# Kernel optimization log

Hardware: AMD Instinct MI355X
Metric: run time of the kernel (lower is better)

## Reference

```python
import jax, jax.numpy as jnp
import numpy as np

B, N = 16, 16          # batch, boxes per image
H, W = 640, 640        # image size
PH, PW = 300, 300      # learned patch size
MIN_AREA = 60.0
MAX_ANG = 20.0 * np.pi / 180.0


def setup_inputs() -> dict:
    key = jax.random.key(0)
    k1, k2, k3 = jax.random.split(key, 3)
    images = jax.random.uniform(k1, (B, H, W, 3), jnp.float32, -1.0, 1.0)
    patch = jax.random.uniform(k2, (PH, PW, 3), jnp.float32, -1.0, 1.0)
    kb1, kb2, kb3 = jax.random.split(k3, 3)
    ymin = jax.random.uniform(kb1, (B, N), jnp.float32, 0.0, H - 220.0)
    xmin = jax.random.uniform(kb2, (B, N), jnp.float32, 0.0, W - 220.0)
    hw = jax.random.uniform(kb3, (B, N, 2), jnp.float32, 100.0, 200.0)
    boxes = jnp.stack([ymin, xmin, ymin + hw[..., 0], xmin + hw[..., 1]], axis=-1)
    scale = jnp.float32(0.4)
    return {"boxes": boxes, "images": images, "patch": patch, "scale": scale}


def _bilinear(img, ys, xs):
    # img [Ph,Pw,3]; ys,xs [H,W] continuous source coords -> [H,W,3]
    Ph, Pw = img.shape[0], img.shape[1]
    y0 = jnp.floor(ys)
    x0 = jnp.floor(xs)
    wy = (ys - y0)[..., None]
    wx = (xs - x0)[..., None]
    y0i = jnp.clip(y0.astype(jnp.int32), 0, Ph - 1)
    y1i = jnp.clip(y0i + 1, 0, Ph - 1)
    x0i = jnp.clip(x0.astype(jnp.int32), 0, Pw - 1)
    x1i = jnp.clip(x0i + 1, 0, Pw - 1)
    v00 = img[y0i, x0i]
    v01 = img[y0i, x1i]
    v10 = img[y1i, x0i]
    v11 = img[y1i, x1i]
    return v00 * (1 - wy) * (1 - wx) + v01 * (1 - wy) * wx + v10 * wy * (1 - wx) + v11 * wy * wx


def _per_image(img, boxes_i, patch, scale, key):
    # random_print_adjust: per-channel affine jitter of the patch
    kw, kb, kloop = jax.random.split(key, 3)
    w = jax.random.normal(kw, (1, 1, 3), jnp.float32) * 0.1 + 0.5
    b = jax.random.normal(kb, (1, 1, 3), jnp.float32) * 0.01
    p = jnp.clip(w * patch + b, -1.0, 1.0)
    # BrightnessMatcher: shift patch mean brightness to match the image
    p = jnp.clip(p + (jnp.mean(img) - jnp.mean(p)), -1.0, 1.0)

    oimg = img
    mask0 = jnp.zeros_like(img)
    yy, xx = jnp.meshgrid(jnp.arange(H, dtype=jnp.float32),
                          jnp.arange(W, dtype=jnp.float32), indexing="ij")

    def step(carry, inp):
        image, mask = carry
        box, kk = inp
        ymin, xmin, ymax, xmax = box[0], box[1], box[2], box[3]
        h = ymax - ymin
        ww = xmax - xmin
        longer = jnp.maximum(h, ww)
        ps = jnp.floor(longer * scale)                       # patch_h == patch_w
        diag = jnp.minimum(jnp.sqrt(2.0).astype(jnp.float32) * ps, jnp.float32(W))
        oy = ymin + h / 2.0
        ox = xmin + ww / 2.0
        y0 = jnp.maximum(oy - diag / 2.0, 0.0)
        x0 = jnp.maximum(ox - diag / 2.0, 0.0)
        y0 = jnp.where(y0 + diag > H, H - diag, y0)
        x0 = jnp.where(x0 + diag > W, W - diag, x0)
        # int casts as in the TF code (values are >= 0, trunc == floor)
        y0i = jnp.floor(y0)
        x0i = jnp.floor(x0)
        phi = jnp.maximum(jnp.floor(ps), 1.0)
        diagi = jnp.floor(diag)
        valid_box = (phi * phi) > MIN_AREA

        k1, k2, k3 = jax.random.split(kk, 3)
        angle = jax.random.uniform(k1, (), jnp.float32, -MAX_ANG, MAX_ANG)

        # inverse warp: output pixel -> padded-patch coords -> resized-patch coords
        u = yy - y0i
        v = xx - x0i
        in_sq = (u >= 0) & (v >= 0) & (u < diagi) & (v < diagi)
        c = (diagi - 1.0) / 2.0
        ca, sa = jnp.cos(angle), jnp.sin(angle)
        su = c + ca * (u - c) - sa * (v - c)
        sv = c + sa * (u - c) + ca * (v - c)
        top = jnp.floor((diagi - phi) / 2.0)   # pad offset (floor top/left)
        py = su - top
        px = sv - top
        valid_src = (py >= 0) & (py <= phi - 1) & (px >= 0) & (px <= phi - 1)
        # resized-patch coords -> original patch coords (bilinear resize, half-pixel)
        sy = (py + 0.5) * (PH / phi) - 0.5
        sx = (px + 0.5) * (PW / phi) - 0.5
        samp = _bilinear(p, sy, sx)                                   # [H,W,3]
        noise = jax.random.uniform(k2, samp.shape, jnp.float32, -0.1, 0.1)
        bright = jax.random.uniform(k3, (), jnp.float32, -0.3, 0.3)
        im = jnp.clip(samp + noise + bright, -1.0, 1.0)
        val = jnp.where(valid_src[..., None], im, -2.0)
        val = jnp.where(val < -1.0, image, val)   # fill with current background
        val = jnp.clip(val, -1.0, 1.0)
        sel = (in_sq & valid_box)[..., None]
        new_image = jnp.where(sel, val, image)
        new_mask = jnp.where(sel, oimg - val, mask)
        return (new_image, new_mask), None

    keys = jax.random.split(kloop, N)
    (img_out, mask_out), _ = jax.lax.scan(step, (img, mask0), (boxes_i, keys))
    return img_out, mask_out


def reference(boxes, images, patch, scale):
    keys = jax.random.split(jax.random.key(42), B)
    img_out, mask_out = jax.vmap(_per_image, in_axes=(0, 0, None, None, 0))(
        images, boxes, patch, scale, keys)
    return img_out, mask_out
```

## Files before the change

### kernel.cpp

```cpp
#include <hip/hip_runtime.h>
#include <stdint.h>
#include <math.h>

#define B_ 16
#define N_ 16
#define H_ 640
#define W_ 640
#define PH_ 300
#define PW_ 300

#define IMG_ELEMS (H_*W_*3)
#define PATCH_ELEMS (PH_*PW_*3)

__device__ __forceinline__ uint2 tf2x32(uint32_t k0, uint32_t k1, uint32_t x0, uint32_t x1) {
  uint32_t k2 = k0 ^ k1 ^ 0x1BD11BDAu;
#define TFR(r) x0 += x1; x1 = (x1 << (r)) | (x1 >> (32 - (r))); x1 ^= x0;
  x0 += k0; x1 += k1;
  TFR(13) TFR(15) TFR(26) TFR(6)
  x0 += k1; x1 += k2 + 1u;
  TFR(17) TFR(29) TFR(16) TFR(24)
  x0 += k2; x1 += k0 + 2u;
  TFR(13) TFR(15) TFR(26) TFR(6)
  x0 += k0; x1 += k1 + 3u;
  TFR(17) TFR(29) TFR(16) TFR(24)
  x0 += k1; x1 += k2 + 4u;
  TFR(13) TFR(15) TFR(26) TFR(6)
  x0 += k2; x1 += k0 + 5u;
#undef TFR
  return make_uint2(x0, x1);
}

__device__ __forceinline__ uint32_t rb32(uint32_t k0, uint32_t k1, uint32_t i) {
  uint2 o = tf2x32(k0, k1, 0u, i);
  return o.x ^ o.y;
}

__device__ __forceinline__ float u01f(uint32_t bits) {
  return __uint_as_float((bits >> 9) | 0x3F800000u) - 1.0f;
}

__device__ __forceinline__ float erfinv32(float x) {
  float w = -log1pf(-x * x);
  float p;
  if (w < 5.0f) {
    w = w - 2.5f;
    p = 2.81022636e-08f;
    p = fmaf(p, w, 3.43273939e-07f);
    p = fmaf(p, w, -3.5233877e-06f);
    p = fmaf(p, w, -4.39150654e-06f);
    p = fmaf(p, w, 0.00021858087f);
    p = fmaf(p, w, -0.00125372503f);
    p = fmaf(p, w, -0.00417768164f);
    p = fmaf(p, w, 0.246640727f);
    p = fmaf(p, w, 1.50140941f);
  } else {
    w = sqrtf(w) - 3.0f;
    p = -0.000200214257f;
    p = fmaf(p, w, 0.000100950558f);
    p = fmaf(p, w, 0.00134934322f);
    p = fmaf(p, w, -0.00367342844f);
    p = fmaf(p, w, 0.00573950773f);
    p = fmaf(p, w, -0.0076224613f);
    p = fmaf(p, w, 0.00943887047f);
    p = fmaf(p, w, 1.00167406f);
    p = fmaf(p, w, 2.83297682f);
  }
  return p * x;
}

__device__ __forceinline__ float jnormal(uint32_t bits) {
  float lo = __uint_as_float(0xBF7FFFFFu);
  float span = 1.0f - lo;
  float u = fmaxf(lo, u01f(bits) * span + lo);
  return 1.4142135623730951f * erfinv32(u);
}

__global__ void setup_kernel(const float* __restrict__ boxes, const float* __restrict__ scale_p,
                             float* __restrict__ params, float* __restrict__ wb) {
  int t = threadIdx.x;
  if (t >= B_*N_) return;
  int b = t >> 4, n = t & 15;
  uint2 kb = tf2x32(0u, 42u, 0u, (uint32_t)b);
  uint2 kw  = tf2x32(kb.x, kb.y, 0u, 0u);
  uint2 kbk = tf2x32(kb.x, kb.y, 0u, 1u);
  uint2 kl  = tf2x32(kb.x, kb.y, 0u, 2u);
  if (n == 0) {
    wb[b*8+0] = jnormal(rb32(kw.x,  kw.y,  0u)) * 0.1f + 0.5f;
    wb[b*8+1] = jnormal(rb32(kw.x,  kw.y,  1u)) * 0.1f + 0.5f;
    wb[b*8+2] = jnormal(rb32(kw.x,  kw.y,  2u)) * 0.1f + 0.5f;
    wb[b*8+3] = jnormal(rb32(kbk.x, kbk.y, 0u)) * 0.01f;
    wb[b*8+4] = jnormal(rb32(kbk.x, kbk.y, 1u)) * 0.01f;
    wb[b*8+5] = jnormal(rb32(kbk.x, kbk.y, 2u)) * 0.01f;
  }
  uint2 kk = tf2x32(kl.x, kl.y, 0u, (uint32_t)n);
  uint2 k1 = tf2x32(kk.x, kk.y, 0u, 0u);
  uint2 k2 = tf2x32(kk.x, kk.y, 0u, 1u);
  uint2 k3 = tf2x32(kk.x, kk.y, 0u, 2u);
  const float MA = (float)(20.0 * 3.14159265358979323846 / 180.0);
  float angle  = fmaxf(-MA,   u01f(rb32(k1.x, k1.y, 0u)) * (MA - (-MA)) + (-MA));
  float bright = fmaxf(-0.3f, u01f(rb32(k3.x, k3.y, 0u)) * (0.3f - (-0.3f)) + (-0.3f));

  const float* bx = boxes + (size_t)t * 4;
  float ymin = bx[0], xmin = bx[1], ymax = bx[2], xmax = bx[3];
  float sc = scale_p[0];
  float h = ymax - ymin, ww = xmax - xmin;
  float longer = fmaxf(h, ww);
  float ps = floorf(longer * sc);
  float diag = fminf(sqrtf(2.0f) * ps, (float)W_);
  float oy = ymin + h * 0.5f;
  float ox = xmin + ww * 0.5f;
  float y0 = fmaxf(oy - diag * 0.5f, 0.0f);
  float x0 = fmaxf(ox - diag * 0.5f, 0.0f);
  if (y0 + diag > (float)H_) y0 = (float)H_ - diag;
  if (x0 + diag > (float)W_) x0 = (float)W_ - diag;
  float y0i = floorf(y0), x0i = floorf(x0);
  float phi = fmaxf(floorf(ps), 1.0f);
  float diagi = floorf(diag);
  float validf = ((phi * phi) > 60.0f) ? 1.0f : 0.0f;
  float c = (diagi - 1.0f) * 0.5f;
  float top = floorf((diagi - phi) * 0.5f);

  float* P = params + t * 16;
  P[0] = y0i; P[1] = x0i; P[2] = diagi; P[3] = phi;
  P[4] = c;
  P[5] = (float)cos((double)angle);
  P[6] = (float)sin((double)angle);
  P[7] = top;
  P[8] = bright; P[9] = (float)PH_ / phi; P[10] = 0.0f; P[11] = validf;
  P[12] = __uint_as_float(k2.x); P[13] = __uint_as_float(k2.y); P[14] = 0.0f; P[15] = 0.0f;
}

__global__ __launch_bounds__(256) void reduce_kernel(
    const float* __restrict__ images, const float* __restrict__ patch,
    const float* __restrict__ wb, double* __restrict__ partials) {
  int b = blockIdx.y, j = blockIdx.x, t = threadIdx.x;
  const float* img = images + (size_t)b * IMG_ELEMS;
  double s = 0.0;
  for (int i = j * 256 + t; i < IMG_ELEMS; i += 64 * 256) s += (double)img[i];
  float w0 = wb[b*8+0], w1 = wb[b*8+1], w2 = wb[b*8+2];
  float b0 = wb[b*8+3], b1 = wb[b*8+4], b2 = wb[b*8+5];
  double sp = 0.0;
  for (int i = j * 256 + t; i < PATCH_ELEMS; i += 64 * 256) {
    int q = i / 3; int ch = i - q * 3;
    float wv = (ch == 0) ? w0 : ((ch == 1) ? w1 : w2);
    float bv = (ch == 0) ? b0 : ((ch == 1) ? b1 : b2);
    float pv = fminf(fmaxf(wv * patch[i] + bv, -1.0f), 1.0f);
    sp += (double)pv;
  }
  __shared__ double sh[256];
  sh[t] = s; __syncthreads();
  for (int o = 128; o > 0; o >>= 1) { if (t < o) sh[t] += sh[t + o]; __syncthreads(); }
  if (t == 0) partials[((size_t)b * 64 + j) * 2 + 0] = sh[0];
  __syncthreads();
  sh[t] = sp; __syncthreads();
  for (int o = 128; o > 0; o >>= 1) { if (t < o) sh[t] += sh[t + o]; __syncthreads(); }
  if (t == 0) partials[((size_t)b * 64 + j) * 2 + 1] = sh[0];
}

__global__ void finalize_kernel(const double* __restrict__ partials, float* __restrict__ dvals) {
  int t = threadIdx.x;
  if (t < B_) {
    double si = 0.0, sp = 0.0;
    for (int j = 0; j < 64; j++) {
      si += partials[((size_t)t * 64 + j) * 2 + 0];
      sp += partials[((size_t)t * 64 + j) * 2 + 1];
    }
    float mi = (float)(si / (double)IMG_ELEMS);
    float mp = (float)(sp / (double)PATCH_ELEMS);
    dvals[t] = mi - mp;
  }
}

__global__ __launch_bounds__(256) void main_kernel(
    const float* __restrict__ images, const float* __restrict__ patch,
    const float* __restrict__ params, const float* __restrict__ wb,
    const float* __restrict__ dvals, float* __restrict__ out) {
  __shared__ float sP[N_ * 16];
  __shared__ float sWB[6];
  __shared__ float sD;
  int b = blockIdx.y;
  int tid = threadIdx.x;
  if (tid < N_ * 16) sP[tid] = params[b * N_ * 16 + tid];
  if (tid < 6) sWB[tid] = wb[b * 8 + tid];
  if (tid == 0) sD = dvals[b];
  __syncthreads();
  int p = blockIdx.x * 256 + tid;
  int y = p / W_;
  int x = p - y * W_;
  size_t base = ((size_t)b * (H_ * W_) + (size_t)p) * 3;
  float orig[3], img[3], mk[3];
#pragma unroll
  for (int ch = 0; ch < 3; ch++) { orig[ch] = images[base + ch]; img[ch] = orig[ch]; mk[ch] = 0.0f; }
  float yf = (float)y, xf = (float)x;
  float dsh = sD;
  for (int n = 0; n < N_; n++) {
    const float* P = sP + n * 16;
    if (P[11] == 0.0f) continue;
    float u = yf - P[0];
    float v = xf - P[1];
    float diagi = P[2];
    if (!(u >= 0.0f && v >= 0.0f && u < diagi && v < diagi)) continue;
    float phi = P[3], c = P[4], ca = P[5], sa = P[6], top = P[7], bright = P[8], sph = P[9];
    float t1 = u - c, t2 = v - c;
    float su = c + ca * t1 - sa * t2;
    float sv = c + sa * t1 + ca * t2;
    float py = su - top;
    float px = sv - top;
    bool vsrc = (py >= 0.0f) && (py <= phi - 1.0f) && (px >= 0.0f) && (px <= phi - 1.0f);
    if (vsrc) {
      float sy = (py + 0.5f) * sph - 0.5f;
      float sx = (px + 0.5f) * sph - 0.5f;
      float fy = floorf(sy), fx = floorf(sx);
      float wy = sy - fy, wxv = sx - fx;
      int iy0 = min(max((int)fy, 0), PH_ - 1);
      int iy1 = min(iy0 + 1, PH_ - 1);
      int ix0 = min(max((int)fx, 0), PW_ - 1);
      int ix1 = min(ix0 + 1, PW_ - 1);
      int o00 = (iy0 * PW_ + ix0) * 3;
      int o01 = (iy0 * PW_ + ix1) * 3;
      int o10 = (iy1 * PW_ + ix0) * 3;
      int o11 = (iy1 * PW_ + ix1) * 3;
      uint32_t k2a = __float_as_uint(P[12]);
      uint32_t k2b = __float_as_uint(P[13]);
      float omwy = 1.0f - wy, omwx = 1.0f - wxv;
      int nbase = p * 3;
#pragma unroll
      for (int ch = 0; ch < 3; ch++) {
        float wv = sWB[ch], bv = sWB[3 + ch];
        float a00 = fminf(fmaxf(wv * patch[o00 + ch] + bv, -1.0f), 1.0f);
        float a01 = fminf(fmaxf(wv * patch[o01 + ch] + bv, -1.0f), 1.0f);
        float a10 = fminf(fmaxf(wv * patch[o10 + ch] + bv, -1.0f), 1.0f);
        float a11 = fminf(fmaxf(wv * patch[o11 + ch] + bv, -1.0f), 1.0f);
        a00 = fminf(fmaxf(a00 + dsh, -1.0f), 1.0f);
        a01 = fminf(fmaxf(a01 + dsh, -1.0f), 1.0f);
        a10 = fminf(fmaxf(a10 + dsh, -1.0f), 1.0f);
        a11 = fminf(fmaxf(a11 + dsh, -1.0f), 1.0f);
        float samp = ((a00 * omwy) * omwx) + ((a01 * omwy) * wxv)
                   + ((a10 * wy) * omwx) + ((a11 * wy) * wxv);
        int i = nbase + ch;
        uint32_t bits = rb32(k2a, k2b, (uint32_t)i);
        float nz = fmaxf(-0.1f, u01f(bits) * (0.1f - (-0.1f)) + (-0.1f));
        float imv = fminf(fmaxf((samp + nz) + bright, -1.0f), 1.0f);
        img[ch] = imv;
        mk[ch] = orig[ch] - imv;
      }
    } else {
#pragma unroll
      for (int ch = 0; ch < 3; ch++) mk[ch] = orig[ch] - img[ch];
    }
  }
  size_t moff = (size_t)B_ * (H_ * W_) * 3;
#pragma unroll
  for (int ch = 0; ch < 3; ch++) {
    out[base + ch] = img[ch];
    out[moff + base + ch] = mk[ch];
  }
}

extern "C" void kernel_launch(void* const* d_in, const int* in_sizes, int n_in,
                              void* d_out, int out_size, void* d_ws, size_t ws_size,
                              hipStream_t stream) {
  const float* boxes  = (const float*)d_in[0];
  const float* images = (const float*)d_in[1];
  const float* patch  = (const float*)d_in[2];
  const float* scale  = (const float*)d_in[3];
  float* out = (float*)d_out;

  float* params = (float*)d_ws;
  float* wb     = params + B_ * N_ * 16;
  float* dvals  = wb + B_ * 8;
  double* partials = (double*)((char*)d_ws + 20480);

  setup_kernel<<<1, 256, 0, stream>>>(boxes, scale, params, wb);
  reduce_kernel<<<dim3(64, B_), 256, 0, stream>>>(images, patch, wb, partials);
  finalize_kernel<<<1, 64, 0, stream>>>(partials, dvals);
  main_kernel<<<dim3((H_ * W_) / 256, B_), 256, 0, stream>>>(images, patch, params, wb, dvals, out);
}
```

Baseline: 302.8 us.

## Vectorize image loads/stores, process 4 pixels per thread, fold finalize into main kernel

The main kernel now has each thread handle 4 consecutive pixels, so it can use three float4 loads and nontemporal float4 stores in place of scalar 3-channel accesses. The reduce kernel reads the image as float4. The separate finalize launch is removed and each main block re-reduces the per-image partials in shared memory to get the brightness shift. This cuts one launch and raises memory transaction width, at the cost of redundant reduction work per block, fewer threads in the grid, and more registers per thread.

```diff
diff --git a/kernel.cpp b/kernel.cpp
--- a/kernel.cpp
+++ b/kernel.cpp
@@ -10,7 +10,10 @@
 #define PW_ 300
 
 #define IMG_ELEMS (H_*W_*3)
+#define IMG_F4    (IMG_ELEMS/4)
 #define PATCH_ELEMS (PH_*PW_*3)
+
+typedef float fx4 __attribute__((ext_vector_type(4)));
 
 __device__ __forceinline__ uint2 tf2x32(uint32_t k0, uint32_t k1, uint32_t x0, uint32_t x1) {
   uint32_t k2 = k0 ^ k1 ^ 0x1BD11BDAu;
@@ -134,9 +137,12 @@
     const float* __restrict__ images, const float* __restrict__ patch,
     const float* __restrict__ wb, double* __restrict__ partials) {
   int b = blockIdx.y, j = blockIdx.x, t = threadIdx.x;
-  const float* img = images + (size_t)b * IMG_ELEMS;
+  const fx4* img4 = (const fx4*)(images + (size_t)b * IMG_ELEMS);
   double s = 0.0;
-  for (int i = j * 256 + t; i < IMG_ELEMS; i += 64 * 256) s += (double)img[i];
+  for (int i = j * 256 + t; i < IMG_F4; i += 64 * 256) {
+    fx4 v = img4[i];
+    s += (double)v.x + (double)v.y + (double)v.z + (double)v.w;
+  }
   float w0 = wb[b*8+0], w1 = wb[b*8+1], w2 = wb[b*8+2];
   float b0 = wb[b*8+3], b1 = wb[b*8+4], b2 = wb[b*8+5];
   double sp = 0.0;
@@ -157,104 +163,127 @@
   if (t == 0) partials[((size_t)b * 64 + j) * 2 + 1] = sh[0];
 }
 
-__global__ void finalize_kernel(const double* __restrict__ partials, float* __restrict__ dvals) {
-  int t = threadIdx.x;
-  if (t < B_) {
-    double si = 0.0, sp = 0.0;
-    for (int j = 0; j < 64; j++) {
-      si += partials[((size_t)t * 64 + j) * 2 + 0];
-      sp += partials[((size_t)t * 64 + j) * 2 + 1];
-    }
-    float mi = (float)(si / (double)IMG_ELEMS);
-    float mp = (float)(sp / (double)PATCH_ELEMS);
-    dvals[t] = mi - mp;
-  }
-}
-
 __global__ __launch_bounds__(256) void main_kernel(
     const float* __restrict__ images, const float* __restrict__ patch,
     const float* __restrict__ params, const float* __restrict__ wb,
-    const float* __restrict__ dvals, float* __restrict__ out) {
+    const double* __restrict__ partials, float* __restrict__ out) {
   __shared__ float sP[N_ * 16];
   __shared__ float sWB[6];
+  __shared__ double sRed[64];
   __shared__ float sD;
   int b = blockIdx.y;
   int tid = threadIdx.x;
   if (tid < N_ * 16) sP[tid] = params[b * N_ * 16 + tid];
   if (tid < 6) sWB[tid] = wb[b * 8 + tid];
-  if (tid == 0) sD = dvals[b];
+  if (tid < 64) {
+    sRed[tid] = partials[((size_t)b * 64 + tid) * 2 + 0];
+  }
   __syncthreads();
-  int p = blockIdx.x * 256 + tid;
-  int y = p / W_;
-  int x = p - y * W_;
-  size_t base = ((size_t)b * (H_ * W_) + (size_t)p) * 3;
-  float orig[3], img[3], mk[3];
+  if (tid < 32) { sRed[tid] += sRed[tid + 32]; }
+  __syncthreads();
+  if (tid == 0) {
+    double si = 0.0;
+    for (int j = 0; j < 32; j++) si += sRed[j];
+    double sp = 0.0;
+    for (int j = 0; j < 64; j++) sp += partials[((size_t)b * 64 + j) * 2 + 1];
+    sD = (float)(si / (double)IMG_ELEMS) - (float)(sp / (double)PATCH_ELEMS);
+  }
+  __syncthreads();
+
+  int g = blockIdx.x * 256 + tid;
+  int p0 = g * 4;
+  int y = p0 / W_;
+  int x0p = p0 - y * W_;
+  size_t base = ((size_t)b * (H_ * W_) + (size_t)p0) * 3;
+  const fx4* in4 = (const fx4*)(images + base);
+  fx4 L0 = in4[0], L1 = in4[1], L2 = in4[2];
+  float pix[12];
+  pix[0]=L0.x; pix[1]=L0.y; pix[2]=L0.z; pix[3]=L0.w;
+  pix[4]=L1.x; pix[5]=L1.y; pix[6]=L1.z; pix[7]=L1.w;
+  pix[8]=L2.x; pix[9]=L2.y; pix[10]=L2.z; pix[11]=L2.w;
+  float img[12], mk[12];
 #pragma unroll
-  for (int ch = 0; ch < 3; ch++) { orig[ch] = images[base + ch]; img[ch] = orig[ch]; mk[ch] = 0.0f; }
-  float yf = (float)y, xf = (float)x;
+  for (int i = 0; i < 12; i++) { img[i] = pix[i]; mk[i] = 0.0f; }
   float dsh = sD;
-  for (int n = 0; n < N_; n++) {
-    const float* P = sP + n * 16;
-    if (P[11] == 0.0f) continue;
-    float u = yf - P[0];
-    float v = xf - P[1];
-    float diagi = P[2];
-    if (!(u >= 0.0f && v >= 0.0f && u < diagi && v < diagi)) continue;
-    float phi = P[3], c = P[4], ca = P[5], sa = P[6], top = P[7], bright = P[8], sph = P[9];
-    float t1 = u - c, t2 = v - c;
-    float su = c + ca * t1 - sa * t2;
-    float sv = c + sa * t1 + ca * t2;
-    float py = su - top;
-    float px = sv - top;
-    bool vsrc = (py >= 0.0f) && (py <= phi - 1.0f) && (px >= 0.0f) && (px <= phi - 1.0f);
-    if (vsrc) {
-      float sy = (py + 0.5f) * sph - 0.5f;
-      float sx = (px + 0.5f) * sph - 0.5f;
-      float fy = floorf(sy), fx = floorf(sx);
-      float wy = sy - fy, wxv = sx - fx;
-      int iy0 = min(max((int)fy, 0), PH_ - 1);
-      int iy1 = min(iy0 + 1, PH_ - 1);
-      int ix0 = min(max((int)fx, 0), PW_ - 1);
-      int ix1 = min(ix0 + 1, PW_ - 1);
-      int o00 = (iy0 * PW_ + ix0) * 3;
-      int o01 = (iy0 * PW_ + ix1) * 3;
-      int o10 = (iy1 * PW_ + ix0) * 3;
-      int o11 = (iy1 * PW_ + ix1) * 3;
-      uint32_t k2a = __float_as_uint(P[12]);
-      uint32_t k2b = __float_as_uint(P[13]);
-      float omwy = 1.0f - wy, omwx = 1.0f - wxv;
-      int nbase = p * 3;
+  float yf = (float)y;
+
 #pragma unroll
-      for (int ch = 0; ch < 3; ch++) {
-        float wv = sWB[ch], bv = sWB[3 + ch];
-        float a00 = fminf(fmaxf(wv * patch[o00 + ch] + bv, -1.0f), 1.0f);
-        float a01 = fminf(fmaxf(wv * patch[o01 + ch] + bv, -1.0f), 1.0f);
-        float a10 = fminf(fmaxf(wv * patch[o10 + ch] + bv, -1.0f), 1.0f);
-        float a11 = fminf(fmaxf(wv * patch[o11 + ch] + bv, -1.0f), 1.0f);
-        a00 = fminf(fmaxf(a00 + dsh, -1.0f), 1.0f);
-        a01 = fminf(fmaxf(a01 + dsh, -1.0f), 1.0f);
-        a10 = fminf(fmaxf(a10 + dsh, -1.0f), 1.0f);
-        a11 = fminf(fmaxf(a11 + dsh, -1.0f), 1.0f);
-        float samp = ((a00 * omwy) * omwx) + ((a01 * omwy) * wxv)
-                   + ((a10 * wy) * omwx) + ((a11 * wy) * wxv);
-        int i = nbase + ch;
-        uint32_t bits = rb32(k2a, k2b, (uint32_t)i);
-        float nz = fmaxf(-0.1f, u01f(bits) * (0.1f - (-0.1f)) + (-0.1f));
-        float imv = fminf(fmaxf((samp + nz) + bright, -1.0f), 1.0f);
-        img[ch] = imv;
-        mk[ch] = orig[ch] - imv;
+  for (int j = 0; j < 4; j++) {
+    float xf = (float)(x0p + j);
+    float* oj = pix + j * 3;
+    float* ij = img + j * 3;
+    float* mj = mk + j * 3;
+    for (int n = 0; n < N_; n++) {
+      const float* P = sP + n * 16;
+      if (P[11] == 0.0f) continue;
+      float u = yf - P[0];
+      float v = xf - P[1];
+      float diagi = P[2];
+      if (!(u >= 0.0f && v >= 0.0f && u < diagi && v < diagi)) continue;
+      float phi = P[3], c = P[4], ca = P[5], sa = P[6], top = P[7], bright = P[8], sph = P[9];
+      float t1 = u - c, t2 = v - c;
+      float su = c + ca * t1 - sa * t2;
+      float sv = c + sa * t1 + ca * t2;
+      float py = su - top;
+      float px = sv - top;
+      bool vsrc = (py >= 0.0f) && (py <= phi - 1.0f) && (px >= 0.0f) && (px <= phi - 1.0f);
+      if (vsrc) {
+        float sy = (py + 0.5f) * sph - 0.5f;
+        float sx = (px + 0.5f) * sph - 0.5f;
+        float fy = floorf(sy), fx = floorf(sx);
+        float wy = sy - fy, wxv = sx - fx;
+        int iy0 = min(max((int)fy, 0), PH_ - 1);
+        int iy1 = min(iy0 + 1, PH_ - 1);
+        int ix0 = min(max((int)fx, 0), PW_ - 1);
+        int ix1 = min(ix0 + 1, PW_ - 1);
+        int o00 = (iy0 * PW_ + ix0) * 3;
+        int o01 = (iy0 * PW_ + ix1) * 3;
+        int o10 = (iy1 * PW_ + ix0) * 3;
+        int o11 = (iy1 * PW_ + ix1) * 3;
+        uint32_t k2a = __float_as_uint(P[12]);
+        uint32_t k2b = __float_as_uint(P[13]);
+        float omwy = 1.0f - wy, omwx = 1.0f - wxv;
+        int nbase = (p0 + j) * 3;
+#pragma unroll
+        for (int ch = 0; ch < 3; ch++) {
+          float wv = sWB[ch], bv = sWB[3 + ch];
+          float a00 = fminf(fmaxf(wv * patch[o00 + ch] + bv, -1.0f), 1.0f);
+          float a01 = fminf(fmaxf(wv * patch[o01 + ch] + bv, -1.0f), 1.0f);
+          float a10 = fminf(fmaxf(wv * patch[o10 + ch] + bv, -1.0f), 1.0f);
+          float a11 = fminf(fmaxf(wv * patch[o11 + ch] + bv, -1.0f), 1.0f);
+          a00 = fminf(fmaxf(a00 + dsh, -1.0f), 1.0f);
+          a01 = fminf(fmaxf(a01 + dsh, -1.0f), 1.0f);
+          a10 = fminf(fmaxf(a10 + dsh, -1.0f), 1.0f);
+          a11 = fminf(fmaxf(a11 + dsh, -1.0f), 1.0f);
+          float samp = ((a00 * omwy) * omwx) + ((a01 * omwy) * wxv)
+                     + ((a10 * wy) * omwx) + ((a11 * wy) * wxv);
+          uint32_t bits = rb32(k2a, k2b, (uint32_t)(nbase + ch));
+          float nz = fmaxf(-0.1f, u01f(bits) * (0.1f - (-0.1f)) + (-0.1f));
+          float imv = fminf(fmaxf((samp + nz) + bright, -1.0f), 1.0f);
+          ij[ch] = imv;
+          mj[ch] = oj[ch] - imv;
+        }
+      } else {
+#pragma unroll
+        for (int ch = 0; ch < 3; ch++) mj[ch] = oj[ch] - ij[ch];
       }
-    } else {
-#pragma unroll
-      for (int ch = 0; ch < 3; ch++) mk[ch] = orig[ch] - img[ch];
     }
   }
   size_t moff = (size_t)B_ * (H_ * W_) * 3;
-#pragma unroll
-  for (int ch = 0; ch < 3; ch++) {
-    out[base + ch] = img[ch];
-    out[moff + base + ch] = mk[ch];
-  }
+  fx4* oi4 = (fx4*)(out + base);
+  fx4* om4 = (fx4*)(out + moff + base);
+  fx4 S0 = {img[0], img[1], img[2],  img[3]};
+  fx4 S1 = {img[4], img[5], img[6],  img[7]};
+  fx4 S2 = {img[8], img[9], img[10], img[11]};
+  fx4 M0 = {mk[0], mk[1], mk[2],  mk[3]};
+  fx4 M1 = {mk[4], mk[5], mk[6],  mk[7]};
+  fx4 M2 = {mk[8], mk[9], mk[10], mk[11]};
+  __builtin_nontemporal_store(S0, oi4 + 0);
+  __builtin_nontemporal_store(S1, oi4 + 1);
+  __builtin_nontemporal_store(S2, oi4 + 2);
+  __builtin_nontemporal_store(M0, om4 + 0);
+  __builtin_nontemporal_store(M1, om4 + 1);
+  __builtin_nontemporal_store(M2, om4 + 2);
 }
 
 extern "C" void kernel_launch(void* const* d_in, const int* in_sizes, int n_in,
@@ -268,11 +297,9 @@
 
   float* params = (float*)d_ws;
   float* wb     = params + B_ * N_ * 16;
-  float* dvals  = wb + B_ * 8;
   double* partials = (double*)((char*)d_ws + 20480);
 
   setup_kernel<<<1, 256, 0, stream>>>(boxes, scale, params, wb);
   reduce_kernel<<<dim3(64, B_), 256, 0, stream>>>(images, patch, wb, partials);
-  finalize_kernel<<<1, 64, 0, stream>>>(partials, dvals);
-  main_kernel<<<dim3((H_ * W_) / 256, B_), 256, 0, stream>>>(images, patch, params, wb, dvals, out);
-}
+  main_kernel<<<dim3((H_ * W_) / (256 * 4), B_), 256, 0, stream>>>(images, patch, params, wb, partials, out);
+}
```

After: 328.7 us. 1.09x slower.
